# Kernel tuning notes

Measured on AMD Instinct MI355X. Metric: run time of the kernel, lower is better.

## Reference

```python
import jax, jax.numpy as jnp
import numpy as np

N = 2048          # total tokens (batch*seq)
H = 4096          # teacher hidden; student hidden = H//2
V = 32000         # vocab
W_HARD = 0.5
W_SOFT = 0.5
BETA = 0.5
IGNORE_INDEX = -100
TEMPERATURE = 2.0


def setup_inputs() -> dict:
    key = jax.random.key(0)
    ks = jax.random.split(key, 7)
    scale_s = 1.0 / np.sqrt(H // 2)
    scale_t = 1.0 / np.sqrt(H)
    return {
        "student_input": jax.random.normal(ks[0], (N, H // 2), jnp.float32),
        "student_weight": jax.random.normal(ks[1], (V, H // 2), jnp.float32) * scale_s,
        "student_bias": jax.random.normal(ks[2], (V,), jnp.float32) * 0.01,
        "teacher_input": jax.random.normal(ks[3], (N, H), jnp.float32),
        "teacher_weight": jax.random.normal(ks[4], (V, H), jnp.float32) * scale_t,
        "teacher_bias": jax.random.normal(ks[5], (V,), jnp.float32) * 0.01,
        "target": jax.random.randint(ks[6], (N,), 0, V, jnp.int64),
    }


def _jsd_lm_head_loss(student_input, student_weight, student_bias,
                      teacher_input, teacher_weight, teacher_bias, target):
    # linear heads: [N, V]
    s_logits = student_input @ student_weight.T + student_bias
    t_logits = teacher_input @ teacher_weight.T + teacher_bias

    n_total = target.shape[0]

    # hard loss: CE on un-tempered student logits, sum over valid, / total tokens
    s_logp_ce = jax.nn.log_softmax(s_logits.astype(jnp.float32), axis=-1)
    valid = target != IGNORE_INDEX
    safe_tgt = jnp.where(valid, target, 0)
    nll = -jnp.take_along_axis(s_logp_ce, safe_tgt[:, None], axis=1)[:, 0]
    hard_loss = jnp.sum(jnp.where(valid, nll, 0.0)) / n_total

    # soft loss: generalized JSD on temperature-scaled logits
    sp = jax.nn.log_softmax((s_logits / TEMPERATURE).astype(jnp.float32), axis=-1)
    tp = jax.nn.log_softmax((t_logits / TEMPERATURE).astype(jnp.float32), axis=-1)
    # mixture m = beta * p_student + (1-beta) * p_teacher (symmetric at beta=0.5)
    log_m = jnp.log(BETA * jnp.exp(sp) + (1.0 - BETA) * jnp.exp(tp))
    kl_s = jnp.sum(jnp.exp(sp) * (sp - log_m))   # KL(student || m), sum-reduced
    kl_t = jnp.sum(jnp.exp(tp) * (tp - log_m))   # KL(teacher || m), sum-reduced
    jsd = BETA * kl_s + (1.0 - BETA) * kl_t
    soft_loss = jsd / n_total

    return W_HARD * hard_loss + W_SOFT * soft_loss


def reference(student_input, student_weight, student_bias,
              teacher_input, teacher_weight, teacher_bias, target):
    return _jsd_lm_head_loss(student_input, student_weight, student_bias,
                             teacher_input, teacher_weight, teacher_bias, target)
```

## Files before the change

kernel.cpp:

```cpp
#include <hip/hip_runtime.h>
#include <hip/hip_bf16.h>
#include <cstdint>
#include <cstddef>

typedef __attribute__((ext_vector_type(8))) short short8v;
typedef __attribute__((ext_vector_type(4))) int   i32x4;

__device__ __forceinline__ short f2bf(float f) {
    union { float f; unsigned u; } c; c.f = f;
    unsigned r = c.u + 0x7FFFu + ((c.u >> 16) & 1u);
    return (short)(r >> 16);
}

__device__ __forceinline__ float bf2f(ushort u) {
    union { unsigned u; float f; } c; c.u = ((unsigned)u) << 16;
    return c.f;
}

__device__ __forceinline__ void load_lds_16B(const void* g, void* l) {
    __builtin_amdgcn_global_load_lds(
        (const __attribute__((address_space(1))) void*)g,
        (__attribute__((address_space(3))) void*)l, 16, 0, 0);
}

__global__ __launch_bounds__(256)
void quant_kernel(const float* __restrict__ src, uint8_t* __restrict__ dst,
                  float* __restrict__ scales, int R, double* accum)
{
    if (accum && blockIdx.x == 0 && threadIdx.x == 0) { accum[0] = 0.0; accum[1] = 0.0; }
    const int r = blockIdx.x;
    const int tid = threadIdx.x;
    const float* x = src + (size_t)r * R;
    const int ng = R >> 10;

    float4 v[4];
    float am = 0.f;
#pragma unroll
    for (int g = 0; g < 4; ++g) {
        if (g < ng) {
            v[g] = *reinterpret_cast<const float4*>(&x[g * 1024 + tid * 4]);
            am = fmaxf(am, fmaxf(fmaxf(fabsf(v[g].x), fabsf(v[g].y)),
                                 fmaxf(fabsf(v[g].z), fabsf(v[g].w))));
        }
    }
#pragma unroll
    for (int off = 32; off > 0; off >>= 1)
        am = fmaxf(am, __shfl_xor(am, off));
    __shared__ float wam[4];
    if ((tid & 63) == 0) wam[tid >> 6] = am;
    __syncthreads();
    am = fmaxf(fmaxf(wam[0], wam[1]), fmaxf(wam[2], wam[3]));
    am = fmaxf(am, 1e-20f);
    const float inv = 127.0f / am;
    if (tid == 0) scales[r] = am / 127.0f;

    uint32_t* out = (uint32_t*)(dst + (size_t)r * R);
#pragma unroll
    for (int g = 0; g < 4; ++g) {
        if (g < ng) {
            int q0 = __float2int_rn(v[g].x * inv);
            int q1 = __float2int_rn(v[g].y * inv);
            int q2 = __float2int_rn(v[g].z * inv);
            int q3 = __float2int_rn(v[g].w * inv);
            q0 = min(127, max(-127, q0)); q1 = min(127, max(-127, q1));
            q2 = min(127, max(-127, q2)); q3 = min(127, max(-127, q3));
            uint32_t pack = (q0 & 255) | ((q1 & 255) << 8) | ((q2 & 255) << 16) | ((uint32_t)(q3 & 255) << 24);
            out[g * 256 + tid] = pack;
        }
    }
}


#define SEG_A0 0
#define SEG_A1 32768
#define SEG_B0 65536
#define SEG_B1 98304

#define READ_B_ALL(bseg) do {                                                  \
    _Pragma("unroll")                                                          \
    for (int nf = 0; nf < 4; ++nf) {                                           \
        const int rb = (bseg) + brow + nf * 2048;                              \
        bfr[nf][0] = *(const i32x4*)&sh[rb + c16a];                            \
        bfr[nf][1] = *(const i32x4*)&sh[rb + c16b];                            \
    }                                                                          \
} while (0)

#define READ_A2(aseg, mfb) do {                                                \
    _Pragma("unroll")                                                          \
    for (int d = 0; d < 2; ++d) {                                              \
        const int ra = (aseg) + arow + ((mfb) + d) * 2048;                     \
        af[d][0] = *(const i32x4*)&sh[ra + c16a];                              \
        af[d][1] = *(const i32x4*)&sh[ra + c16b];                              \
    }                                                                          \
} while (0)

#define MFMA16(mfb) do {                                                       \
    __builtin_amdgcn_s_setprio(1);                                             \
    _Pragma("unroll")                                                          \
    for (int d = 0; d < 2; ++d) {                                              \
        _Pragma("unroll")                                                      \
        for (int nf = 0; nf < 4; ++nf) {                                       \
            acc[(mfb)+d][nf] = __builtin_amdgcn_mfma_i32_16x16x64_i8(          \
                af[d][0], bfr[nf][0], acc[(mfb)+d][nf], 0, 0, 0);              \
            acc[(mfb)+d][nf] = __builtin_amdgcn_mfma_i32_16x16x64_i8(          \
                af[d][1], bfr[nf][1], acc[(mfb)+d][nf], 0, 0, 0);              \
        }                                                                      \
    }                                                                          \
    __builtin_amdgcn_s_setprio(0);                                             \
} while (0)

#define BAR() __builtin_amdgcn_s_barrier()
#define VMCNT4() asm volatile("s_waitcnt vmcnt(4)" ::: "memory")
#define VMCNT0() asm volatile("s_waitcnt vmcnt(0)" ::: "memory")

__global__ __launch_bounds__(512, 2)
void gemm256_i8_kernel(const uint8_t* __restrict__ A, const uint8_t* __restrict__ W,
                       const float* __restrict__ sa, const float* __restrict__ sw,
                       const float* __restrict__ bias, ushort* __restrict__ C,
                       int K, int V)
{
    __shared__ uint8_t sh[131072];
    ushort* shs = (ushort*)sh;

    const int tid  = threadIdx.x;
    const int lane = tid & 63;
    const int wave = tid >> 6;
    const int wm = wave >> 2;
    const int wn = wave & 3;

    const int cpx = gridDim.x >> 3;
    const int wg  = ((int)blockIdx.x & 7) * cpx + ((int)blockIdx.x >> 3);
    const int row0 = (wg & 7) * 256;
    const int col0 = (wg >> 3) * 256;

    const int NT = K >> 7;
    const int NI = NT >> 1;

    const int sr  = lane >> 3;
    const int scb = ((lane & 7) ^ sr) * 16;
    const size_t a_off = (size_t)(row0 + wave * 8 + sr) * K + scb;
    const size_t w_off = (size_t)(col0 + wave * 8 + sr) * K + scb;
    const int lds_u = wave * 1024;

    auto stage_half = [&](const uint8_t* gb, size_t goff, int seg, int h, int k0) {
        const uint8_t* g0 = gb + goff + (size_t)(h * 128) * K + k0;
        load_lds_16B(g0,                  &sh[seg + h * 16384 + lds_u]);
        load_lds_16B(g0 + (size_t)64 * K, &sh[seg + h * 16384 + 8192 + lds_u]);
    };

    const int l15  = lane & 15;
    const int c16a = (((lane >> 4)    ) ^ (lane & 7)) * 16;
    const int c16b = (((lane >> 4) + 4) ^ (lane & 7)) * 16;
    const int arow = (wm * 128 + l15) * 128;
    const int brow = (wn * 64  + l15) * 128;

    i32x4 acc[8][4];
#pragma unroll
    for (int m = 0; m < 8; ++m)
#pragma unroll
        for (int n = 0; n < 4; ++n)
            acc[m][n] = (i32x4)(0);

    i32x4 bfr[4][2];
    i32x4 af[2][2];

    stage_half(A, a_off, SEG_A0, 0, 0);
    stage_half(A, a_off, SEG_A0, 1, 0);
    stage_half(W, w_off, SEG_B0, 0, 0);
    stage_half(W, w_off, SEG_B0, 1, 0);
    stage_half(W, w_off, SEG_B1, 0, 128);
    stage_half(W, w_off, SEG_B1, 1, 128);
    VMCNT4();
    BAR();

    for (int i = 0; i < NI - 1; ++i) {
        const int kA1 = (2 * i + 1) * 128;
        const int kN2 = (2 * i + 2) * 128;
        const int kB3 = (2 * i + 3) * 128;

        READ_B_ALL(SEG_B0); READ_A2(SEG_A0, 0);
        stage_half(A, a_off, SEG_A1, 0, kA1);
        BAR(); MFMA16(0); BAR();

        READ_A2(SEG_A0, 2);
        stage_half(A, a_off, SEG_A1, 1, kA1);
        BAR(); MFMA16(2); BAR();

        READ_A2(SEG_A0, 4);
        stage_half(W, w_off, SEG_B0, 0, kN2);
        BAR(); MFMA16(4); BAR();

        READ_A2(SEG_A0, 6);
        stage_half(W, w_off, SEG_B0, 1, kN2);
        BAR(); MFMA16(6);
        VMCNT4();
        BAR();

        READ_B_ALL(SEG_B1); READ_A2(SEG_A1, 0);
        stage_half(A, a_off, SEG_A0, 0, kN2);
        BAR(); MFMA16(0); BAR();

        READ_A2(SEG_A1, 2);
        stage_half(A, a_off, SEG_A0, 1, kN2);
        BAR(); MFMA16(2); BAR();

        READ_A2(SEG_A1, 4);
        stage_half(W, w_off, SEG_B1, 0, kB3);
        BAR(); MFMA16(4); BAR();

        READ_A2(SEG_A1, 6);
        stage_half(W, w_off, SEG_B1, 1, kB3);
        BAR(); MFMA16(6);
        VMCNT4();
        BAR();
    }

    {
        const int kA1 = (NT - 1) * 128;
        READ_B_ALL(SEG_B0); READ_A2(SEG_A0, 0);
        stage_half(A, a_off, SEG_A1, 0, kA1);
        BAR(); MFMA16(0); BAR();
        READ_A2(SEG_A0, 2);
        stage_half(A, a_off, SEG_A1, 1, kA1);
        BAR(); MFMA16(2); BAR();
        READ_A2(SEG_A0, 4); BAR(); MFMA16(4); BAR();
        READ_A2(SEG_A0, 6); BAR(); MFMA16(6);
        VMCNT0();
        BAR();
        READ_B_ALL(SEG_B1); READ_A2(SEG_A1, 0); BAR(); MFMA16(0); BAR();
        READ_A2(SEG_A1, 2); BAR(); MFMA16(2); BAR();
        READ_A2(SEG_A1, 4); BAR(); MFMA16(4); BAR();
        READ_A2(SEG_A1, 6); BAR(); MFMA16(6);
    }

    float bb[4], swv[4];
#pragma unroll
    for (int nf = 0; nf < 4; ++nf) {
        const int gc = col0 + wn * 64 + nf * 16 + l15;
        bb[nf]  = bias[gc];
        swv[nf] = sw[gc];
    }

    __syncthreads();
#pragma unroll
    for (int mf = 0; mf < 8; ++mf) {
        const int rl = wm * 128 + mf * 16 + (lane >> 4) * 4;
        const float4 sav = *reinterpret_cast<const float4*>(&sa[row0 + rl]);
        const float* savp = (const float*)&sav;
#pragma unroll
        for (int nf = 0; nf < 4; ++nf) {
            const int cl = wn * 64 + nf * 16 + l15;
#pragma unroll
            for (int j = 0; j < 4; ++j) {
                const int row = rl + j;
                const float v = (float)acc[mf][nf][j] * (savp[j] * swv[nf]) + bb[nf];
                const int pc = (((cl >> 3) ^ (((row >> 2) & 3) << 1)) << 3) + (cl & 7);
                shs[row * 256 + pc] = (ushort)f2bf(v);
            }
        }
    }
    __syncthreads();
#pragma unroll
    for (int pass = 0; pass < 16; ++pass) {
        const int r = pass * 16 + (tid >> 5);
        const int pc16 = (tid & 31) ^ (((r >> 2) & 3) << 1);
        *reinterpret_cast<short8v*>(&C[(size_t)(row0 + r) * V + col0 + (tid & 31) * 8]) =
            *reinterpret_cast<const short8v*>(&shs[r * 256 + pc16 * 8]);
    }
}

__global__ __launch_bounds__(1024)
void stats_loss_kernel(const ushort* __restrict__ S, const ushort* __restrict__ Tm,
                       const int* __restrict__ tgt, double* __restrict__ accum, int V)
{
    const int r = blockIdx.x;
    const ushort* s = S  + (size_t)r * V;
    const ushort* t = Tm + (size_t)r * V;
    const int tid = threadIdx.x;

    short8v sv[4], tv[4];
    bool valid[4];

    float ms = -1e30f, l1 = 0.f, lh = 0.f;
    float mt = -1e30f, lt = 0.f;
#pragma unroll
    for (int it = 0; it < 4; ++it) {
        const int v = it * 8192 + tid * 8;
        valid[it] = (v < V);
        if (valid[it]) {
            sv[it] = *reinterpret_cast<const short8v*>(&s[v]);
            tv[it] = *reinterpret_cast<const short8v*>(&t[v]);
#pragma unroll
            for (int j = 0; j < 8; ++j) {
                float x = bf2f((ushort)sv[it][j]);
                if (x > ms) {
                    float eh = __expf(0.5f * (ms - x));
                    lh *= eh; l1 *= eh * eh; ms = x;
                }
                float e = __expf(0.5f * (x - ms));
                lh += e; l1 += e * e;
                float y = bf2f((ushort)tv[it][j]);
                if (y > mt) {
                    lt *= __expf(0.5f * (mt - y));
                    mt = y;
                }
                lt += __expf(0.5f * (y - mt));
            }
        }
    }
#pragma unroll
    for (int off = 32; off > 0; off >>= 1) {
        float mso = __shfl_xor(ms, off), l1o = __shfl_xor(l1, off), lho = __shfl_xor(lh, off);
        float mn = fmaxf(ms, mso);
        float ea = __expf(0.5f * (ms - mn)), eb = __expf(0.5f * (mso - mn));
        lh = lh * ea + lho * eb;
        l1 = l1 * ea * ea + l1o * eb * eb;
        ms = mn;
        float mto = __shfl_xor(mt, off), lto = __shfl_xor(lt, off);
        float mn2 = fmaxf(mt, mto);
        lt = lt * __expf(0.5f * (mt - mn2)) + lto * __expf(0.5f * (mto - mn2));
        mt = mn2;
    }
    __shared__ float red[16][5];
    __shared__ float bc[3];
    if ((tid & 63) == 0) {
        int w = tid >> 6;
        red[w][0] = ms; red[w][1] = l1; red[w][2] = lh;
        red[w][3] = mt; red[w][4] = lt;
    }
    __syncthreads();
    if (tid == 0) {
        float M = red[0][0], L1 = red[0][1], LH = red[0][2];
        float Mt = red[0][3], Lt = red[0][4];
#pragma unroll
        for (int w = 1; w < 16; ++w) {
            float mn = fmaxf(M, red[w][0]);
            float ea = __expf(0.5f * (M - mn)), eb = __expf(0.5f * (red[w][0] - mn));
            LH = LH * ea + red[w][2] * eb;
            L1 = L1 * ea * ea + red[w][1] * eb * eb;
            M = mn;
            float mn2 = fmaxf(Mt, red[w][3]);
            Lt = Lt * __expf(0.5f * (Mt - mn2)) + red[w][4] * __expf(0.5f * (red[w][3] - mn2));
            Mt = mn2;
        }
        bc[0] = M + __logf(L1);
        bc[1] = 0.5f * M + __logf(LH);
        bc[2] = 0.5f * Mt + __logf(Lt);
    }
    __syncthreads();
    const float ls1 = bc[0], ls2 = bc[1], lt2 = bc[2];

    float local = 0.f;
#pragma unroll
    for (int it = 0; it < 4; ++it) {
        if (valid[it]) {
#pragma unroll
            for (int j = 0; j < 8; ++j) {
                float sp = 0.5f * bf2f((ushort)sv[it][j]) - ls2;
                float tp = 0.5f * bf2f((ushort)tv[it][j]) - lt2;
                float p = __expf(sp), q = __expf(tp);
                float mm = 0.5f * (p + q);
                float lm = __logf(fmaxf(mm, 1e-38f));
                local += 0.5f * (p * (sp - lm) + q * (tp - lm));
            }
        }
    }
#pragma unroll
    for (int off = 32; off > 0; off >>= 1)
        local += __shfl_xor(local, off);
    __shared__ float ls[16];
    if ((tid & 63) == 0) ls[tid >> 6] = local;
    __syncthreads();
    if (tid == 0) {
        float blocksum = 0.f;
#pragma unroll
        for (int w = 0; w < 16; ++w) blocksum += ls[w];
        atomicAdd(&accum[1], (double)blocksum);
        int tg = tgt[r];
        if (tg != -100) {
            float nll = -(bf2f(s[tg]) - ls1);
            atomicAdd(&accum[0], (double)nll);
        }
    }
}

__global__ void finalize_kernel(const double* __restrict__ accum,
                                float* __restrict__ out, double inv_n) {
    out[0] = (float)(0.5 * (accum[0] * inv_n) + 0.5 * (accum[1] * inv_n));
}

extern "C" void kernel_launch(void* const* d_in, const int* in_sizes, int n_in,
                              void* d_out, int out_size, void* d_ws, size_t ws_size,
                              hipStream_t stream)
{
    const float* s_in = (const float*)d_in[0];
    const float* s_w  = (const float*)d_in[1];
    const float* s_b  = (const float*)d_in[2];
    const float* t_in = (const float*)d_in[3];
    const float* t_w  = (const float*)d_in[4];
    const float* t_b  = (const float*)d_in[5];
    const int*   tgt  = (const int*)d_in[6];

    const int N = 2048, V = 32000, KS = 2048, KT = 4096;

    const size_t e_sin = (size_t)N * KS;
    const size_t e_sw  = (size_t)V * KS;
    const size_t e_tin = (size_t)N * KT;
    const size_t e_tw  = (size_t)V * KT;

    char* ws = (char*)d_ws;
    double* accum = (double*)ws;

    float* sa_s = (float*)(ws + 4096);
    float* sa_t = sa_s + 2048;
    float* sw_s = sa_t + 2048;
    float* sw_t = sw_s + 32000;
    uint8_t* s_in_q = (uint8_t*)(ws + 278528);
    uint8_t* s_w_q  = s_in_q + e_sin;
    uint8_t* t_in_q = s_w_q + e_sw;
    uint8_t* t_w_q  = t_in_q + e_tin;
    ushort* s_log = (ushort*)(t_w_q + e_tw);
    ushort* t_log = s_log + (size_t)N * V;

    quant_kernel<<<N, 256, 0, stream>>>(s_in, s_in_q, sa_s, KS, accum);
    quant_kernel<<<N, 256, 0, stream>>>(t_in, t_in_q, sa_t, KT, nullptr);
    quant_kernel<<<V, 256, 0, stream>>>(s_w, s_w_q, sw_s, KS, nullptr);
    quant_kernel<<<V, 256, 0, stream>>>(t_w, t_w_q, sw_t, KT, nullptr);

    const int grid = (V / 256) * (N / 256);
    gemm256_i8_kernel<<<grid, 512, 0, stream>>>(s_in_q, s_w_q, sa_s, sw_s, s_b, s_log, KS, V);
    gemm256_i8_kernel<<<grid, 512, 0, stream>>>(t_in_q, t_w_q, sa_t, sw_t, t_b, t_log, KT, V);

    stats_loss_kernel<<<N, 1024, 0, stream>>>(s_log, t_log, tgt, accum, V);

    finalize_kernel<<<1, 1, 0, stream>>>(accum, (float*)d_out, 1.0 / (double)N);
}
```

Before: 721.2 us.

## Merge quant launches, fuse dual GEMMs, store logits as FP8 e4m3

The four quantization launches become one kernel that picks its source by block index. The student and teacher int8 GEMMs run as a single interleaved launch, so the shorter student tiles fill gaps and tail effects shrink. Logits are now written as FP8 e4m3 instead of bf16, which halves logit write and read traffic in the GEMM epilogue and the loss kernel. The cost is a large precision loss on logits (3 mantissa bits), which may push the loss outside tolerance, plus extra conversion ALU work.

```diff
diff --git a/kernel.cpp b/kernel.cpp
--- a/kernel.cpp
+++ b/kernel.cpp
@@ -17,6 +17,36 @@
     return c.f;
 }
 
+__device__ __forceinline__ uint32_t f32_to_e4m3(float x) {
+    union { float f; uint32_t u; } c; c.f = x;
+    uint32_t s = (c.u >> 31) << 7;
+    float ax = fabsf(x);
+    if (ax < 0.015625f) {
+        int q = __float2int_rn(ax * 512.0f);
+        return s | (uint32_t)q;
+    }
+    if (ax >= 464.0f) return s | 0x7E;
+    union { float f; uint32_t u; } a; a.f = ax;
+    uint32_t lsb = (a.u >> 20) & 1;
+    uint32_t u = a.u + 0x7FFFF + lsb;
+    uint32_t E = ((u >> 23) & 255) - 120;
+    uint32_t m = (u >> 20) & 7;
+    return s | (E << 3) | m;
+}
+
+__device__ __forceinline__ float e4m3_to_f32(uint32_t b) {
+    uint32_t E = (b >> 3) & 15, m = b & 7;
+    float v;
+    if (E == 0) {
+        v = (float)m * 0.001953125f;
+    } else {
+        union { uint32_t u; float f; } c;
+        c.u = ((E + 120) << 23) | (m << 20);
+        v = c.f;
+    }
+    return (b & 0x80) ? -v : v;
+}
+
 __device__ __forceinline__ void load_lds_16B(const void* g, void* l) {
     __builtin_amdgcn_global_load_lds(
         (const __attribute__((address_space(1))) void*)g,
@@ -24,13 +54,25 @@
 }
 
 __global__ __launch_bounds__(256)
-void quant_kernel(const float* __restrict__ src, uint8_t* __restrict__ dst,
-                  float* __restrict__ scales, int R, double* accum)
+void quant_all_kernel(const float* __restrict__ s_in, const float* __restrict__ t_in,
+                      const float* __restrict__ s_w,  const float* __restrict__ t_w,
+                      uint8_t* __restrict__ s_in_q, uint8_t* __restrict__ t_in_q,
+                      uint8_t* __restrict__ s_w_q,  uint8_t* __restrict__ t_w_q,
+                      float* __restrict__ sa_s, float* __restrict__ sa_t,
+                      float* __restrict__ sw_s, float* __restrict__ sw_t,
+                      double* __restrict__ accum)
 {
-    if (accum && blockIdx.x == 0 && threadIdx.x == 0) { accum[0] = 0.0; accum[1] = 0.0; }
-    const int r = blockIdx.x;
+    const int b = blockIdx.x;
+    if (b == 0 && threadIdx.x == 0) { accum[0] = 0.0; accum[1] = 0.0; }
+
+    const float* src; uint8_t* dst; float* sc; int R, row;
+    if (b < 2048)       { src = s_in; dst = s_in_q; sc = sa_s; R = 2048; row = b; }
+    else if (b < 4096)  { src = t_in; dst = t_in_q; sc = sa_t; R = 4096; row = b - 2048; }
+    else if (b < 36096) { src = s_w;  dst = s_w_q;  sc = sw_s; R = 2048; row = b - 4096; }
+    else                { src = t_w;  dst = t_w_q;  sc = sw_t; R = 4096; row = b - 36096; }
+
     const int tid = threadIdx.x;
-    const float* x = src + (size_t)r * R;
+    const float* x = src + (size_t)row * R;
     const int ng = R >> 10;
 
     float4 v[4];
@@ -52,9 +94,9 @@
     am = fmaxf(fmaxf(wam[0], wam[1]), fmaxf(wam[2], wam[3]));
     am = fmaxf(am, 1e-20f);
     const float inv = 127.0f / am;
-    if (tid == 0) scales[r] = am / 127.0f;
-
-    uint32_t* out = (uint32_t*)(dst + (size_t)r * R);
+    if (tid == 0) sc[row] = am / 127.0f;
+
+    uint32_t* out = (uint32_t*)(dst + (size_t)row * R);
 #pragma unroll
     for (int g = 0; g < 4; ++g) {
         if (g < ng) {
@@ -64,8 +106,8 @@
             int q3 = __float2int_rn(v[g].w * inv);
             q0 = min(127, max(-127, q0)); q1 = min(127, max(-127, q1));
             q2 = min(127, max(-127, q2)); q3 = min(127, max(-127, q3));
-            uint32_t pack = (q0 & 255) | ((q1 & 255) << 8) | ((q2 & 255) << 16) | ((uint32_t)(q3 & 255) << 24);
-            out[g * 256 + tid] = pack;
+            out[g * 256 + tid] = (q0 & 255) | ((q1 & 255) << 8) |
+                                 ((q2 & 255) << 16) | ((uint32_t)(q3 & 255) << 24);
         }
     }
 }
@@ -114,10 +156,13 @@
 #define VMCNT0() asm volatile("s_waitcnt vmcnt(0)" ::: "memory")
 
 __global__ __launch_bounds__(512, 2)
-void gemm256_i8_kernel(const uint8_t* __restrict__ A, const uint8_t* __restrict__ W,
-                       const float* __restrict__ sa, const float* __restrict__ sw,
-                       const float* __restrict__ bias, ushort* __restrict__ C,
-                       int K, int V)
+void gemm256_i8_dual_kernel(const uint8_t* __restrict__ At, const uint8_t* __restrict__ Wt,
+                            const float* __restrict__ sat, const float* __restrict__ swt,
+                            const float* __restrict__ bt,  uint8_t* __restrict__ Ct,
+                            const uint8_t* __restrict__ As, const uint8_t* __restrict__ Ws,
+                            const float* __restrict__ sas, const float* __restrict__ sws,
+                            const float* __restrict__ bs,  uint8_t* __restrict__ Cs,
+                            int V)
 {
     __shared__ uint8_t sh[131072];
     ushort* shs = (ushort*)sh;
@@ -129,9 +174,17 @@
     const int wn = wave & 3;
 
     const int cpx = gridDim.x >> 3;
-    const int wg  = ((int)blockIdx.x & 7) * cpx + ((int)blockIdx.x >> 3);
-    const int row0 = (wg & 7) * 256;
-    const int col0 = (wg >> 3) * 256;
+    const int wgid = ((int)blockIdx.x & 7) * cpx + ((int)blockIdx.x >> 3);
+    const int w  = wgid >> 1;
+    const bool teacher = (wgid & 1) == 0;
+
+    const uint8_t* A; const uint8_t* W; const float* sa; const float* sw;
+    const float* bias; uint8_t* C; int K;
+    if (teacher) { A = At; W = Wt; sa = sat; sw = swt; bias = bt; C = Ct; K = 4096; }
+    else         { A = As; W = Ws; sa = sas; sw = sws; bias = bs; C = Cs; K = 2048; }
+
+    const int row0 = (w & 7) * 256;
+    const int col0 = (w >> 3) * 256;
 
     const int NT = K >> 7;
     const int NI = NT >> 1;
@@ -253,9 +306,9 @@
 #pragma unroll
             for (int j = 0; j < 4; ++j) {
                 const int row = rl + j;
-                const float v = (float)acc[mf][nf][j] * (savp[j] * swv[nf]) + bb[nf];
+                const float vv = (float)acc[mf][nf][j] * (savp[j] * swv[nf]) + bb[nf];
                 const int pc = (((cl >> 3) ^ (((row >> 2) & 3) << 1)) << 3) + (cl & 7);
-                shs[row * 256 + pc] = (ushort)f2bf(v);
+                shs[row * 256 + pc] = (ushort)f2bf(vv);
             }
         }
     }
@@ -264,21 +317,29 @@
     for (int pass = 0; pass < 16; ++pass) {
         const int r = pass * 16 + (tid >> 5);
         const int pc16 = (tid & 31) ^ (((r >> 2) & 3) << 1);
-        *reinterpret_cast<short8v*>(&C[(size_t)(row0 + r) * V + col0 + (tid & 31) * 8]) =
-            *reinterpret_cast<const short8v*>(&shs[r * 256 + pc16 * 8]);
+        short8v vv = *reinterpret_cast<const short8v*>(&shs[r * 256 + pc16 * 8]);
+        uint32_t b0 = 0, b1 = 0;
+#pragma unroll
+        for (int j = 0; j < 4; ++j)
+            b0 |= f32_to_e4m3(bf2f((ushort)vv[j])) << (8 * j);
+#pragma unroll
+        for (int j = 4; j < 8; ++j)
+            b1 |= f32_to_e4m3(bf2f((ushort)vv[j])) << (8 * (j - 4));
+        uint2 o; o.x = b0; o.y = b1;
+        *reinterpret_cast<uint2*>(&C[(size_t)(row0 + r) * V + col0 + (tid & 31) * 8]) = o;
     }
 }
 
 __global__ __launch_bounds__(1024)
-void stats_loss_kernel(const ushort* __restrict__ S, const ushort* __restrict__ Tm,
+void stats_loss_kernel(const uint8_t* __restrict__ S, const uint8_t* __restrict__ Tm,
                        const int* __restrict__ tgt, double* __restrict__ accum, int V)
 {
     const int r = blockIdx.x;
-    const ushort* s = S  + (size_t)r * V;
-    const ushort* t = Tm + (size_t)r * V;
+    const uint8_t* s = S  + (size_t)r * V;
+    const uint8_t* t = Tm + (size_t)r * V;
     const int tid = threadIdx.x;
 
-    short8v sv[4], tv[4];
+    uint2 sv[4], tv[4];
     bool valid[4];
 
     float ms = -1e30f, l1 = 0.f, lh = 0.f;
@@ -288,18 +349,20 @@
         const int v = it * 8192 + tid * 8;
         valid[it] = (v < V);
         if (valid[it]) {
-            sv[it] = *reinterpret_cast<const short8v*>(&s[v]);
-            tv[it] = *reinterpret_cast<const short8v*>(&t[v]);
+            sv[it] = *reinterpret_cast<const uint2*>(&s[v]);
+            tv[it] = *reinterpret_cast<const uint2*>(&t[v]);
 #pragma unroll
             for (int j = 0; j < 8; ++j) {
-                float x = bf2f((ushort)sv[it][j]);
+                uint32_t sb = (j < 4 ? (sv[it].x >> (8 * j)) : (sv[it].y >> (8 * (j - 4)))) & 255u;
+                uint32_t tb = (j < 4 ? (tv[it].x >> (8 * j)) : (tv[it].y >> (8 * (j - 4)))) & 255u;
+                float x = e4m3_to_f32(sb);
                 if (x > ms) {
                     float eh = __expf(0.5f * (ms - x));
                     lh *= eh; l1 *= eh * eh; ms = x;
                 }
                 float e = __expf(0.5f * (x - ms));
                 lh += e; l1 += e * e;
-                float y = bf2f((ushort)tv[it][j]);
+                float y = e4m3_to_f32(tb);
                 if (y > mt) {
                     lt *= __expf(0.5f * (mt - y));
                     mt = y;
@@ -324,23 +387,23 @@
     __shared__ float red[16][5];
     __shared__ float bc[3];
     if ((tid & 63) == 0) {
-        int w = tid >> 6;
-        red[w][0] = ms; red[w][1] = l1; red[w][2] = lh;
-        red[w][3] = mt; red[w][4] = lt;
+        int wv = tid >> 6;
+        red[wv][0] = ms; red[wv][1] = l1; red[wv][2] = lh;
+        red[wv][3] = mt; red[wv][4] = lt;
     }
     __syncthreads();
     if (tid == 0) {
         float M = red[0][0], L1 = red[0][1], LH = red[0][2];
         float Mt = red[0][3], Lt = red[0][4];
 #pragma unroll
-        for (int w = 1; w < 16; ++w) {
-            float mn = fmaxf(M, red[w][0]);
-            float ea = __expf(0.5f * (M - mn)), eb = __expf(0.5f * (red[w][0] - mn));
-            LH = LH * ea + red[w][2] * eb;
-            L1 = L1 * ea * ea + red[w][1] * eb * eb;
+        for (int wv = 1; wv < 16; ++wv) {
+            float mn = fmaxf(M, red[wv][0]);
+            float ea = __expf(0.5f * (M - mn)), eb = __expf(0.5f * (red[wv][0] - mn));
+            LH = LH * ea + red[wv][2] * eb;
+            L1 = L1 * ea * ea + red[wv][1] * eb * eb;
             M = mn;
-            float mn2 = fmaxf(Mt, red[w][3]);
-            Lt = Lt * __expf(0.5f * (Mt - mn2)) + red[w][4] * __expf(0.5f * (red[w][3] - mn2));
+            float mn2 = fmaxf(Mt, red[wv][3]);
+            Lt = Lt * __expf(0.5f * (Mt - mn2)) + red[wv][4] * __expf(0.5f * (red[wv][3] - mn2));
             Mt = mn2;
         }
         bc[0] = M + __logf(L1);
@@ -356,8 +419,10 @@
         if (valid[it]) {
 #pragma unroll
             for (int j = 0; j < 8; ++j) {
-                float sp = 0.5f * bf2f((ushort)sv[it][j]) - ls2;
-                float tp = 0.5f * bf2f((ushort)tv[it][j]) - lt2;
+                uint32_t sb = (j < 4 ? (sv[it].x >> (8 * j)) : (sv[it].y >> (8 * (j - 4)))) & 255u;
+                uint32_t tb = (j < 4 ? (tv[it].x >> (8 * j)) : (tv[it].y >> (8 * (j - 4)))) & 255u;
+                float sp = 0.5f * e4m3_to_f32(sb) - ls2;
+                float tp = 0.5f * e4m3_to_f32(tb) - lt2;
                 float p = __expf(sp), q = __expf(tp);
                 float mm = 0.5f * (p + q);
                 float lm = __logf(fmaxf(mm, 1e-38f));
@@ -374,11 +439,11 @@
     if (tid == 0) {
         float blocksum = 0.f;
 #pragma unroll
-        for (int w = 0; w < 16; ++w) blocksum += ls[w];
+        for (int wv = 0; wv < 16; ++wv) blocksum += ls[wv];
         atomicAdd(&accum[1], (double)blocksum);
         int tg = tgt[r];
         if (tg != -100) {
-            float nll = -(bf2f(s[tg]) - ls1);
+            float nll = -(e4m3_to_f32(s[tg]) - ls1);
             atomicAdd(&accum[0], (double)nll);
         }
     }
@@ -419,17 +484,18 @@
     uint8_t* s_w_q  = s_in_q + e_sin;
     uint8_t* t_in_q = s_w_q + e_sw;
     uint8_t* t_w_q  = t_in_q + e_tin;
-    ushort* s_log = (ushort*)(t_w_q + e_tw);
-    ushort* t_log = s_log + (size_t)N * V;
-
-    quant_kernel<<<N, 256, 0, stream>>>(s_in, s_in_q, sa_s, KS, accum);
-    quant_kernel<<<N, 256, 0, stream>>>(t_in, t_in_q, sa_t, KT, nullptr);
-    quant_kernel<<<V, 256, 0, stream>>>(s_w, s_w_q, sw_s, KS, nullptr);
-    quant_kernel<<<V, 256, 0, stream>>>(t_w, t_w_q, sw_t, KT, nullptr);
-
-    const int grid = (V / 256) * (N / 256);
-    gemm256_i8_kernel<<<grid, 512, 0, stream>>>(s_in_q, s_w_q, sa_s, sw_s, s_b, s_log, KS, V);
-    gemm256_i8_kernel<<<grid, 512, 0, stream>>>(t_in_q, t_w_q, sa_t, sw_t, t_b, t_log, KT, V);
+    uint8_t* s_log = t_w_q + e_tw;
+    uint8_t* t_log = s_log + (size_t)N * V;
+
+    quant_all_kernel<<<68096, 256, 0, stream>>>(
+        s_in, t_in, s_w, t_w,
+        s_in_q, t_in_q, s_w_q, t_w_q,
+        sa_s, sa_t, sw_s, sw_t, accum);
+
+    const int grid = 2 * (V / 256) * (N / 256);
+    gemm256_i8_dual_kernel<<<grid, 512, 0, stream>>>(
+        t_in_q, t_w_q, sa_t, sw_t, t_b, t_log,
+        s_in_q, s_w_q, sa_s, sw_s, s_b, s_log, V);
 
     stats_loss_kernel<<<N, 1024, 0, stream>>>(s_log, t_log, tgt, accum, V);
 
```

Measured after the change: 831.1 us. +15.2%, slower.
